# Performance work log

Hardware: AMD Instinct MI355X
Metric: run time of the kernel (lower is better)

The kernel has to match this reference:

```python
import jax, jax.numpy as jnp
import numpy as np

B, C, H, W = 4, 256, 64, 64
RED = 8
DQK = C // RED  # 32


def setup_inputs() -> dict:
    key = jax.random.key(0)
    ks = jax.random.split(key, 8)
    x = jax.random.normal(ks[0], (B, C, H, W), dtype=jnp.float32)
    # 1x1 conv weights == per-pixel linear maps: [out_ch, in_ch] + bias [out_ch]
    q_w = jax.random.normal(ks[1], (DQK, C), dtype=jnp.float32) * (1.0 / np.sqrt(C))
    q_b = jax.random.normal(ks[2], (DQK,), dtype=jnp.float32) * 0.01
    k_w = jax.random.normal(ks[3], (DQK, C), dtype=jnp.float32) * (1.0 / np.sqrt(C))
    k_b = jax.random.normal(ks[4], (DQK,), dtype=jnp.float32) * 0.01
    v_w = jax.random.normal(ks[5], (C, C), dtype=jnp.float32) * (1.0 / np.sqrt(C))
    v_b = jax.random.normal(ks[6], (C,), dtype=jnp.float32) * 0.01
    # gamma is init'd to 0 in torch; use a nonzero value so the attention path matters
    gamma = jax.random.normal(ks[7], (1,), dtype=jnp.float32) * 0.1
    return {"x": x, "q_w": q_w, "q_b": q_b, "k_w": k_w, "k_b": k_b,
            "v_w": v_w, "v_b": v_b, "gamma": gamma}


def reference(x, q_w, q_b, k_w, k_b, v_w, v_b, gamma):
    b, c, h, w = x.shape
    xf = x.reshape(b, c, h * w)  # [B, C, N]
    # 1x1 convs as channel matmuls
    q = jnp.einsum('dc,bcn->bdn', q_w, xf) + q_b[None, :, None]  # [B, DQK, N]
    k = jnp.einsum('dc,bcn->bdn', k_w, xf) + k_b[None, :, None]  # [B, DQK, N]
    v = jnp.einsum('oc,bcn->bon', v_w, xf) + v_b[None, :, None]  # [B, C, N]
    # attn[b, n, m] = softmax_m( q[:,n] . k[:,m] )  -- NO 1/sqrt(d) scale (faithful)
    scores = jnp.einsum('bdn,bdm->bnm', q, k)  # [B, N, N]
    attn = jax.nn.softmax(scores, axis=-1)
    # out = v @ attn^T : out[b, c, n] = sum_m v[b, c, m] * attn[b, n, m]
    out = jnp.einsum('bcm,bnm->bcn', v, attn).reshape(b, c, h, w)
    return gamma[0] * out + x
```

## Files before the change

kernel.cpp:

```cpp
#include <hip/hip_runtime.h>

#define NN 4096
#define CC 256
#define DQ 32

typedef __attribute__((ext_vector_type(8))) short short8;
typedef __attribute__((ext_vector_type(4))) short short4v;
typedef __attribute__((ext_vector_type(4))) float f32x4;

__device__ __forceinline__ unsigned short f32_to_bf16(float f) {
  unsigned int u = __float_as_uint(f);
  u += 0x7fffu + ((u >> 16) & 1u);
  return (unsigned short)(u >> 16);
}

__device__ __forceinline__ float exp2_hw(float f) {
  return __builtin_amdgcn_exp2f(f);
}

__device__ __forceinline__ void gld16(const void* g, void* l) {
  __builtin_amdgcn_global_load_lds(
      (__attribute__((address_space(1))) void*)(g),
      (__attribute__((address_space(3))) void*)(l), 16, 0, 0);
}

__global__ __launch_bounds__(256) void wconv_kernel(
    const float* qw, const float* kw, const float* vw,
    const float* qb, const float* kb, const float* vb,
    unsigned short* Wcat, float* bcat) {
  int id = blockIdx.x * 256 + threadIdx.x;
  if (id < 320 * 256) {
    int row = id >> 8;
    float v;
    if (row < 32) v = qw[id];
    else if (row < 64) v = kw[id - 32 * 256];
    else v = vw[id - 64 * 256];
    Wcat[id] = f32_to_bf16(v);
  }
  if (id < 320) {
    float v;
    if (id < 32) v = qb[id];
    else if (id < 64) v = kb[id - 32];
    else v = vb[id - 64];
    bcat[id] = v;
  }
}

__global__ __launch_bounds__(256) void xpose_kernel(const float* x, unsigned short* xbT) {
  int bid = blockIdx.x;
  int b = bid >> 8, cb = (bid >> 6) & 3, nb = bid & 63;
  __shared__ float tile[64][65];
  int lane = threadIdx.x & 63, r4 = threadIdx.x >> 6;
  const float* xp = x + (((size_t)b * CC + cb * 64) * NN) + nb * 64;
#pragma unroll
  for (int p = 0; p < 16; p++) {
    int c = p * 4 + r4;
    tile[c][lane] = xp[(size_t)c * NN + lane];
  }
  __syncthreads();
  unsigned short* dp = xbT + (((size_t)b * NN + nb * 64) * CC) + cb * 64;
#pragma unroll
  for (int p = 0; p < 16; p++) {
    int n = p * 4 + r4;
    dp[(size_t)n * CC + lane] = f32_to_bf16(tile[lane][n]);
  }
}

__global__ __launch_bounds__(256) void proj_kernel(
    const unsigned short* xbT, const unsigned short* Wcat, const float* bcat,
    unsigned short* Qt, unsigned short* Kt, unsigned short* V) {
  int bid = blockIdx.x;
  int b = bid >> 6, nb = bid & 63;
  int tid = threadIdx.x, lane = tid & 63, w = tid >> 6;
  int l15 = lane & 15, h = lane >> 4;
  int n0 = nb * 64 + w * 16;
  const unsigned short* xp = xbT + (size_t)b * NN * CC;

  short8 af[8];
#pragma unroll
  for (int ks = 0; ks < 8; ks++)
    af[ks] = *(const short8*)(xp + (size_t)(n0 + l15) * CC + ks * 32 + h * 8);

  f32x4 acc[20];
#pragma unroll
  for (int t = 0; t < 20; t++)
#pragma unroll
    for (int r = 0; r < 4; r++) acc[t][r] = 0.f;

#pragma unroll
  for (int ks = 0; ks < 8; ks++) {
#pragma unroll
    for (int dt = 0; dt < 20; dt++) {
      short8 bfr = *(const short8*)(Wcat + (size_t)(dt * 16 + l15) * CC + ks * 32 + h * 8);
      acc[dt] = __builtin_amdgcn_mfma_f32_16x16x32_bf16(af[ks], bfr, acc[dt], 0, 0, 0);
    }
  }

  unsigned short* Qtb = Qt + (size_t)b * NN * DQ;
  unsigned short* Ktb = Kt + (size_t)b * NN * DQ;
#pragma unroll
  for (int dt = 0; dt < 4; dt++) {
    float bias = bcat[dt * 16 + l15];
    float scale = dt < 2 ? 1.44269504f : 1.0f;
    unsigned short* dst = dt < 2 ? Qtb : Ktb;
    int dd = (dt & 1) * 16 + l15;
#pragma unroll
    for (int r = 0; r < 4; r++) {
      int n = n0 + h * 4 + r;
      dst[(size_t)n * DQ + dd] = f32_to_bf16((acc[dt][r] + bias) * scale);
    }
  }

  __shared__ unsigned short vbuf[CC][64];
#pragma unroll
  for (int dt = 4; dt < 20; dt++) {
    float bias = bcat[dt * 16 + l15];
    int c = (dt - 4) * 16 + l15;
#pragma unroll
    for (int r = 0; r < 4; r++) {
      int nl = w * 16 + h * 4 + r;
      vbuf[c][nl] = f32_to_bf16(acc[dt][r] + bias);
    }
  }
  __syncthreads();
  unsigned short* Vb = V + (size_t)b * CC * NN + nb * 64;
  for (int cc = 0; cc < 64; cc++) {
    int c = w * 64 + cc;
    Vb[(size_t)c * NN + lane] = vbuf[c][lane];
  }
}

__global__ __launch_bounds__(512) void attn_kernel(
    const unsigned short* Qt, const unsigned short* Kt, const unsigned short* V,
    const float* x, const float* gamma, float* out) {
  int bid = blockIdx.x;
  int b = (bid & 7) >> 1;
  int nb = (bid >> 3) * 2 + (bid & 1);
  int tid = threadIdx.x, lane = tid & 63, w = tid >> 6;
  int grp = w >> 2;
  int wq = w & 3;
  int l15 = lane & 15, h = lane >> 4;
  int n0 = nb * 64 + wq * 16;

  const unsigned short* Qtb = Qt + (size_t)b * NN * DQ;
  const unsigned short* Ktb = Kt + (size_t)b * NN * DQ;
  const unsigned short* Vb  = V  + (size_t)b * CC * NN;

  __shared__ __align__(16) unsigned short vbuf[4][CC * 64];
  __shared__ __align__(16) unsigned short pbuf[8][16 * 64];
  __shared__ float sstat[8][32];

  short8 qf = *(const short8*)(Qtb + (size_t)(n0 + l15) * DQ + h * 8);

  f32x4 acc[16];
#pragma unroll
  for (int t = 0; t < 16; t++)
#pragma unroll
    for (int r = 0; r < 4; r++) acc[t][r] = 0.f;
  float run_max = -1e30f, rs = 0.f;

  f32x4 zero4;
#pragma unroll
  for (int r = 0; r < 4; r++) zero4[r] = 0.f;

  auto stageSS = [&](int t) {
#pragma unroll
    for (int ch = 0; ch < 2; ch++) {
      int ck = 2 * t + ch;
      int m0 = ck * 64;
      char* dst = (char*)&vbuf[ck & 3][0];
#pragma unroll
      for (int it = 0; it < 4; it++) {
        int idx = it * 512 + tid;
        int c = idx >> 3, sub = idx & 7;
        int moff = (sub ^ (c & 7)) * 8;
        gld16(Vb + (size_t)c * NN + m0 + moff, dst + idx * 16);
      }
    }
  };

#define KLOAD(T, KF) do { int ci_ = 2 * (T) + grp; \
  _Pragma("unroll") for (int s_ = 0; s_ < 4; s_++) \
    KF[s_] = *(const short8*)(Ktb + (size_t)(ci_ * 64 + s_ * 16 + l15) * DQ + h * 8); \
} while (0)

  short8 kA[4], kB[4];
  stageSS(0);
  KLOAD(0, kA);

#define SUPERSTEP(T, KF, KN) do { \
  __syncthreads();   \
  if ((T) + 1 < 32) stageSS((T) + 1); \
  f32x4 st[4]; \
  _Pragma("unroll") for (int s = 0; s < 4; s++) \
    st[s] = __builtin_amdgcn_mfma_f32_16x16x32_bf16(KF[s], qf, zero4, 0, 0, 0); \
  if ((T) + 1 < 32) KLOAD((T) + 1, KN); \
  float cmax = -1e30f; \
  _Pragma("unroll") for (int s = 0; s < 4; s++) \
    _Pragma("unroll") for (int r = 0; r < 4; r++) cmax = fmaxf(cmax, st[s][r]); \
  cmax = fmaxf(cmax, __shfl_xor(cmax, 16)); \
  cmax = fmaxf(cmax, __shfl_xor(cmax, 32)); \
  if (__any(cmax > run_max + 8.0f)) { \
    float nm = fmaxf(run_max, cmax); \
    float sc = exp2_hw(run_max - nm); \
    rs *= sc; \
    _Pragma("unroll") for (int t_ = 0; t_ < 16; t_++) \
      _Pragma("unroll") for (int r = 0; r < 4; r++) acc[t_][r] *= sc; \
    run_max = nm; \
  } \
  float lsum = 0.f; \
  unsigned short pu[16]; \
  _Pragma("unroll") for (int s = 0; s < 4; s++) \
    _Pragma("unroll") for (int r = 0; r < 4; r++) { \
      float p = exp2_hw(st[s][r] - run_max); \
      lsum += p; \
      pu[s * 4 + r] = f32_to_bf16(p); \
    } \
  rs += lsum; \
  char* pb = (char*)&pbuf[w][0]; \
  _Pragma("unroll") for (int s = 0; s < 4; s++) { \
    short4v pv; \
    _Pragma("unroll") for (int r = 0; r < 4; r++) pv[r] = (short)pu[s * 4 + r]; \
    int inner = (s * 32 + h * 8) ^ ((l15 & 7) << 4); \
    *(short4v*)(pb + l15 * 128 + inner) = pv; \
  } \
  const char* vb2 = (const char*)&vbuf[(2 * (T) + grp) & 3][0]; \
  __builtin_amdgcn_s_setprio(1); \
  _Pragma("unroll") for (int p = 0; p < 2; p++) { \
    int pinner = (p * 64 + h * 16) ^ ((l15 & 7) << 4); \
    short8 pf = *(const short8*)(pb + l15 * 128 + pinner); \
    _Pragma("unroll") for (int ct = 0; ct < 16; ct++) { \
      int c = ct * 16 + l15; \
      int sub = (p * 4 + h) ^ (c & 7); \
      short8 vf = *(const short8*)(vb2 + c * 128 + sub * 16); \
      acc[ct] = __builtin_amdgcn_mfma_f32_16x16x32_bf16(vf, pf, acc[ct], 0, 0, 0); \
    } \
  } \
  __builtin_amdgcn_s_setprio(0); \
} while (0)

  for (int t2 = 0; t2 < 16; t2++) {
    SUPERSTEP(2 * t2, kA, kB);
    SUPERSTEP(2 * t2 + 1, kB, kA);
  }
#undef SUPERSTEP
#undef KLOAD

  rs += __shfl_xor(rs, 16);
  rs += __shfl_xor(rs, 32);

  __syncthreads();
  float* sacc = (float*)&vbuf[0][0];
  if (grp == 0) {
#pragma unroll
    for (int j = 0; j < 8; j++)
      *(f32x4*)(sacc + (size_t)w * 2048 + j * 256 + lane * 4) = acc[8 + j];
  } else {
#pragma unroll
    for (int j = 0; j < 8; j++)
      *(f32x4*)(sacc + (size_t)w * 2048 + j * 256 + lane * 4) = acc[j];
  }
  if (h == 0) { sstat[w][l15 * 2] = run_max; sstat[w][l15 * 2 + 1] = rs; }
  __syncthreads();

  int pw = w ^ 4;
  float m_p = sstat[pw][l15 * 2], rs_p = sstat[pw][l15 * 2 + 1];
  float nm = fmaxf(run_max, m_p);
  float s_own = exp2_hw(run_max - nm), s_p = exp2_hw(m_p - nm);
  float rstot = rs * s_own + rs_p * s_p;
  float inv = 1.0f / rstot;
  float g = gamma[0];
  const float* xb = x + (size_t)b * CC * NN;
  float* ob = out + (size_t)b * CC * NN;

  if (grp == 0) {
#pragma unroll
    for (int j = 0; j < 8; j++) {
      f32x4 ap = *(const f32x4*)(sacc + (size_t)pw * 2048 + j * 256 + lane * 4);
#pragma unroll
      for (int r = 0; r < 4; r++) {
        int c = j * 16 + h * 4 + r;
        size_t off = (size_t)c * NN + n0 + l15;
        ob[off] = g * (acc[j][r] * s_own + ap[r] * s_p) * inv + xb[off];
      }
    }
  } else {
#pragma unroll
    for (int j = 0; j < 8; j++) {
      f32x4 ap = *(const f32x4*)(sacc + (size_t)pw * 2048 + j * 256 + lane * 4);
#pragma unroll
      for (int r = 0; r < 4; r++) {
        int c = (8 + j) * 16 + h * 4 + r;
        size_t off = (size_t)c * NN + n0 + l15;
        ob[off] = g * (acc[8 + j][r] * s_own + ap[r] * s_p) * inv + xb[off];
      }
    }
  }
}

extern "C" void kernel_launch(void* const* d_in, const int* in_sizes, int n_in,
                              void* d_out, int out_size, void* d_ws, size_t ws_size,
                              hipStream_t stream) {
  (void)in_sizes; (void)n_in; (void)out_size; (void)ws_size;
  const float* x  = (const float*)d_in[0];
  const float* qw = (const float*)d_in[1];
  const float* qb = (const float*)d_in[2];
  const float* kw = (const float*)d_in[3];
  const float* kb = (const float*)d_in[4];
  const float* vw = (const float*)d_in[5];
  const float* vb = (const float*)d_in[6];
  const float* gamma = (const float*)d_in[7];
  float* out = (float*)d_out;

  char* ws = (char*)d_ws;
  unsigned short* xbT  = (unsigned short*)(ws);
  unsigned short* Wcat = (unsigned short*)(ws + 8388608);
  float*          bcat = (float*)(ws + 8388608 + 163840);
  unsigned short* Qt   = (unsigned short*)(ws + 8553728);
  unsigned short* Kt   = (unsigned short*)(ws + 9602304);
  unsigned short* V    = (unsigned short*)(ws + 10650880);

  hipLaunchKernelGGL(wconv_kernel, dim3(320), dim3(256), 0, stream,
                     qw, kw, vw, qb, kb, vb, Wcat, bcat);
  hipLaunchKernelGGL(xpose_kernel, dim3(1024), dim3(256), 0, stream, x, xbT);
  hipLaunchKernelGGL(proj_kernel, dim3(256), dim3(256), 0, stream,
                     xbT, Wcat, bcat, Qt, Kt, V);
  hipLaunchKernelGGL(attn_kernel, dim3(256), dim3(512), 0, stream,
                     Qt, Kt, V, x, gamma, out);
}
```

Measured before the change: 109.1 us.

## Repartition PV matmul so each wave owns a channel slice across all query rows

Before, each wave computed all 256 output channels for its own 16 query rows. Now the four waves in a group share their P tiles through LDS after an added barrier, and each wave computes a 64-channel slice for all 64 query rows, so every loaded V fragment feeds four MFMAs. Because rescaling now needs every row's scale factor, each superstep publishes per-row scales to LDS and applies them to the matching accumulators. The epilogue reduces over both groups: group 1 writes its partials to LDS and group 0 combines them and writes the output. The cost is an extra barrier per superstep and more P reads from LDS.

```diff
diff --git a/kernel.cpp b/kernel.cpp
--- a/kernel.cpp
+++ b/kernel.cpp
@@ -139,6 +139,7 @@
   int tid = threadIdx.x, lane = tid & 63, w = tid >> 6;
   int grp = w >> 2;
   int wq = w & 3;
+  int wc = w & 3;
   int l15 = lane & 15, h = lane >> 4;
   int n0 = nb * 64 + wq * 16;
 
@@ -149,6 +150,7 @@
   __shared__ __align__(16) unsigned short vbuf[4][CC * 64];
   __shared__ __align__(16) unsigned short pbuf[8][16 * 64];
   __shared__ float sstat[8][32];
+  __shared__ float sscale[8][16];
 
   short8 qf = *(const short8*)(Qtb + (size_t)(n0 + l15) * DQ + h * 8);
 
@@ -200,12 +202,11 @@
     _Pragma("unroll") for (int r = 0; r < 4; r++) cmax = fmaxf(cmax, st[s][r]); \
   cmax = fmaxf(cmax, __shfl_xor(cmax, 16)); \
   cmax = fmaxf(cmax, __shfl_xor(cmax, 32)); \
+  float sc_ = 1.0f; \
   if (__any(cmax > run_max + 8.0f)) { \
     float nm = fmaxf(run_max, cmax); \
-    float sc = exp2_hw(run_max - nm); \
-    rs *= sc; \
-    _Pragma("unroll") for (int t_ = 0; t_ < 16; t_++) \
-      _Pragma("unroll") for (int r = 0; r < 4; r++) acc[t_][r] *= sc; \
+    sc_ = exp2_hw(run_max - nm); \
+    rs *= sc_; \
     run_max = nm; \
   } \
   float lsum = 0.f; \
@@ -217,26 +218,48 @@
       pu[s * 4 + r] = f32_to_bf16(p); \
     } \
   rs += lsum; \
-  char* pb = (char*)&pbuf[w][0]; \
+  { char* pb = (char*)&pbuf[w][0]; \
   _Pragma("unroll") for (int s = 0; s < 4; s++) { \
     short4v pv; \
     _Pragma("unroll") for (int r = 0; r < 4; r++) pv[r] = (short)pu[s * 4 + r]; \
     int inner = (s * 32 + h * 8) ^ ((l15 & 7) << 4); \
     *(short4v*)(pb + l15 * 128 + inner) = pv; \
-  } \
-  const char* vb2 = (const char*)&vbuf[(2 * (T) + grp) & 3][0]; \
+  } } \
+  if (h == 0) sscale[w][l15] = sc_; \
+   \
+  asm volatile("s_waitcnt lgkmcnt(0)" ::: "memory"); \
+  __builtin_amdgcn_s_barrier(); \
+  asm volatile("" ::: "memory"); \
+  { float scv0 = sscale[grp * 4 + 0][l15]; \
+    float scv1 = sscale[grp * 4 + 1][l15]; \
+    float scv2 = sscale[grp * 4 + 2][l15]; \
+    float scv3 = sscale[grp * 4 + 3][l15]; \
+    if (__any(scv0 != 1.0f || scv1 != 1.0f || scv2 != 1.0f || scv3 != 1.0f)) { \
+      _Pragma("unroll") for (int ct = 0; ct < 4; ct++) \
+        _Pragma("unroll") for (int r = 0; r < 4; r++) { \
+          acc[ct * 4 + 0][r] *= scv0; acc[ct * 4 + 1][r] *= scv1; \
+          acc[ct * 4 + 2][r] *= scv2; acc[ct * 4 + 3][r] *= scv3; \
+        } \
+    } } \
+  { const char* vb2 = (const char*)&vbuf[(2 * (T) + grp) & 3][0]; \
   __builtin_amdgcn_s_setprio(1); \
   _Pragma("unroll") for (int p = 0; p < 2; p++) { \
     int pinner = (p * 64 + h * 16) ^ ((l15 & 7) << 4); \
-    short8 pf = *(const short8*)(pb + l15 * 128 + pinner); \
-    _Pragma("unroll") for (int ct = 0; ct < 16; ct++) { \
-      int c = ct * 16 + l15; \
+    short8 pf0 = *(const short8*)((const char*)&pbuf[grp * 4 + 0][0] + l15 * 128 + pinner); \
+    short8 pf1 = *(const short8*)((const char*)&pbuf[grp * 4 + 1][0] + l15 * 128 + pinner); \
+    short8 pf2 = *(const short8*)((const char*)&pbuf[grp * 4 + 2][0] + l15 * 128 + pinner); \
+    short8 pf3 = *(const short8*)((const char*)&pbuf[grp * 4 + 3][0] + l15 * 128 + pinner); \
+    _Pragma("unroll") for (int ct = 0; ct < 4; ct++) { \
+      int c = wc * 64 + ct * 16 + l15; \
       int sub = (p * 4 + h) ^ (c & 7); \
       short8 vf = *(const short8*)(vb2 + c * 128 + sub * 16); \
-      acc[ct] = __builtin_amdgcn_mfma_f32_16x16x32_bf16(vf, pf, acc[ct], 0, 0, 0); \
+      acc[ct * 4 + 0] = __builtin_amdgcn_mfma_f32_16x16x32_bf16(vf, pf0, acc[ct * 4 + 0], 0, 0, 0); \
+      acc[ct * 4 + 1] = __builtin_amdgcn_mfma_f32_16x16x32_bf16(vf, pf1, acc[ct * 4 + 1], 0, 0, 0); \
+      acc[ct * 4 + 2] = __builtin_amdgcn_mfma_f32_16x16x32_bf16(vf, pf2, acc[ct * 4 + 2], 0, 0, 0); \
+      acc[ct * 4 + 3] = __builtin_amdgcn_mfma_f32_16x16x32_bf16(vf, pf3, acc[ct * 4 + 3], 0, 0, 0); \
     } \
   } \
-  __builtin_amdgcn_s_setprio(0); \
+  __builtin_amdgcn_s_setprio(0); } \
 } while (0)
 
   for (int t2 = 0; t2 < 16; t2++) {
@@ -248,53 +271,45 @@
 
   rs += __shfl_xor(rs, 16);
   rs += __shfl_xor(rs, 32);
-
-  __syncthreads();
-  float* sacc = (float*)&vbuf[0][0];
-  if (grp == 0) {
-#pragma unroll
-    for (int j = 0; j < 8; j++)
-      *(f32x4*)(sacc + (size_t)w * 2048 + j * 256 + lane * 4) = acc[8 + j];
-  } else {
-#pragma unroll
-    for (int j = 0; j < 8; j++)
-      *(f32x4*)(sacc + (size_t)w * 2048 + j * 256 + lane * 4) = acc[j];
-  }
   if (h == 0) { sstat[w][l15 * 2] = run_max; sstat[w][l15 * 2 + 1] = rs; }
   __syncthreads();
 
-  int pw = w ^ 4;
-  float m_p = sstat[pw][l15 * 2], rs_p = sstat[pw][l15 * 2 + 1];
-  float nm = fmaxf(run_max, m_p);
-  float s_own = exp2_hw(run_max - nm), s_p = exp2_hw(m_p - nm);
-  float rstot = rs * s_own + rs_p * s_p;
-  float inv = 1.0f / rstot;
-  float g = gamma[0];
-  const float* xb = x + (size_t)b * CC * NN;
-  float* ob = out + (size_t)b * CC * NN;
+  float* sacc = (float*)&vbuf[0][0];
+  if (grp == 1) {
+#pragma unroll
+    for (int ct = 0; ct < 4; ct++)
+#pragma unroll
+      for (int nt = 0; nt < 4; nt++)
+        *(f32x4*)(sacc + ((wc * 16 + ct * 4 + nt) << 8) + lane * 4) = acc[ct * 4 + nt];
+  }
+  __syncthreads();
 
   if (grp == 0) {
-#pragma unroll
-    for (int j = 0; j < 8; j++) {
-      f32x4 ap = *(const f32x4*)(sacc + (size_t)pw * 2048 + j * 256 + lane * 4);
-#pragma unroll
-      for (int r = 0; r < 4; r++) {
-        int c = j * 16 + h * 4 + r;
-        size_t off = (size_t)c * NN + n0 + l15;
-        ob[off] = g * (acc[j][r] * s_own + ap[r] * s_p) * inv + xb[off];
+    float g = gamma[0];
+    float s0v[4], s1v[4], invv[4];
+#pragma unroll
+    for (int nt = 0; nt < 4; nt++) {
+      float m0 = sstat[nt][l15 * 2],     r0 = sstat[nt][l15 * 2 + 1];
+      float m1 = sstat[4 + nt][l15 * 2], r1 = sstat[4 + nt][l15 * 2 + 1];
+      float nm = fmaxf(m0, m1);
+      float s0 = exp2_hw(m0 - nm), s1 = exp2_hw(m1 - nm);
+      s0v[nt] = s0; s1v[nt] = s1;
+      invv[nt] = 1.0f / (r0 * s0 + r1 * s1);
+    }
+    const float* xb = x + (size_t)b * CC * NN;
+    float* ob = out + (size_t)b * CC * NN;
+#pragma unroll
+    for (int ct = 0; ct < 4; ct++)
+#pragma unroll
+      for (int nt = 0; nt < 4; nt++) {
+        f32x4 ap = *(const f32x4*)(sacc + ((wc * 16 + ct * 4 + nt) << 8) + lane * 4);
+#pragma unroll
+        for (int r = 0; r < 4; r++) {
+          int c = wc * 64 + ct * 16 + h * 4 + r;
+          size_t off = (size_t)c * NN + (size_t)nb * 64 + nt * 16 + l15;
+          ob[off] = g * (acc[ct * 4 + nt][r] * s0v[nt] + ap[r] * s1v[nt]) * invv[nt] + xb[off];
+        }
       }
-    }
-  } else {
-#pragma unroll
-    for (int j = 0; j < 8; j++) {
-      f32x4 ap = *(const f32x4*)(sacc + (size_t)pw * 2048 + j * 256 + lane * 4);
-#pragma unroll
-      for (int r = 0; r < 4; r++) {
-        int c = (8 + j) * 16 + h * 4 + r;
-        size_t off = (size_t)c * NN + n0 + l15;
-        ob[off] = g * (acc[8 + j][r] * s_own + ap[r] * s_p) * inv + xb[off];
-      }
-    }
   }
 }
 
```

New measurement: 111.4 us. 1.02x slower.
